# Kernel optimization log

Measured on AMD Instinct MI355X. Metric: run time of the kernel, lower is better.

## Reference

```python
import jax, jax.numpy as jnp
import numpy as np

BATCH = 2048
INPUT_DIM = 512
N = 8 ** 4  # reservoir_n ** reservoir_d = 4096
T = 16
NEG_SLOPE = 0.1
SPARSITY = 0.1  # fraction of nonzero entries in the pre-trained reservoir W


def setup_inputs() -> dict:
    key = jax.random.key(0)
    kx, kw, km = jax.random.split(key, 3)
    x = jax.random.normal(kx, (BATCH, INPUT_DIM), dtype=jnp.float32)
    # Sparse pre-trained reservoir weights; scale keeps spectral norm ~O(1)
    # so the T-step recurrence neither explodes nor vanishes.
    mask = (jax.random.uniform(km, (N, N)) < SPARSITY).astype(jnp.float32)
    W = jax.random.normal(kw, (N, N), dtype=jnp.float32) * mask / jnp.sqrt(SPARSITY * N)
    return {"x": x, "W": W}


def reference(x, W):
    # Pad input [B, input_dim] -> initial state S [B, N]
    S0 = jnp.pad(x, ((0, 0), (0, N - x.shape[1])))

    def step(S, _):
        S = jax.nn.leaky_relu(S @ W, negative_slope=NEG_SLOPE)
        return S, None

    S_final, _ = jax.lax.scan(step, S0, None, length=T)
    return S_final
```

## Files before the change

### kernel.cpp

```cpp
#include <hip/hip_runtime.h>


#define BATCH 2048
#define NDIM  4096
#define INDIM 512
#define BM 128
#define BN 128
#define BK 32

typedef _Float16 f16x8 __attribute__((ext_vector_type(8)));
typedef float    f32x4 __attribute__((ext_vector_type(4)));

__device__ __forceinline__ void async16(const void* gsrc, void* ldst) {
  const __attribute__((address_space(1))) unsigned int* g =
      (const __attribute__((address_space(1))) unsigned int*)gsrc;
  __attribute__((address_space(3))) unsigned int* l =
      (__attribute__((address_space(3))) unsigned int*)ldst;
  __builtin_amdgcn_global_load_lds(g, l, 16, 0, 0);
}

__global__ void prep_x(const float* __restrict__ x,
                       _Float16* __restrict__ Sh, _Float16* __restrict__ Sl) {
  size_t i = (size_t)blockIdx.x * 256 + threadIdx.x;
  int b = (int)(i >> 12);
  int n = (int)(i & (NDIM - 1));
  float v = (n < INDIM) ? x[(size_t)b * INDIM + n] : 0.0f;
  _Float16 h = (_Float16)v;
  Sh[i] = h;
  Sl[i] = (_Float16)(v - (float)h);
}

__global__ void prep_w(const float* __restrict__ W,
                       _Float16* __restrict__ Wth, _Float16* __restrict__ Wtl) {
  __shared__ float tile[32][33];
  int k0 = blockIdx.y * 32, n0 = blockIdx.x * 32;
  int tx = threadIdx.x, ty = threadIdx.y;
  for (int r = 0; r < 4; r++) {
    int k = k0 + ty + r * 8;
    tile[ty + r * 8][tx] = W[(size_t)k * NDIM + n0 + tx];
  }
  __syncthreads();
  for (int r = 0; r < 4; r++) {
    int n = n0 + ty + r * 8;
    float v = tile[tx][ty + r * 8] * 256.0f;
    _Float16 h = (_Float16)v;
    Wth[(size_t)n * NDIM + k0 + tx] = h;
    Wtl[(size_t)n * NDIM + k0 + tx] = (_Float16)(v - (float)h);
  }
}

#define READF(b, A, L, Bv, M)                          \
  do {                                                 \
    _Pragma("unroll") for (int i = 0; i < 4; i++) {    \
      A[i]  = *(const f16x8*)&sAh[b][oA[i]];           \
      L[i]  = *(const f16x8*)&sAl[b][oA[i]];           \
      Bv[i] = *(const f16x8*)&sBh[b][oB[i]];           \
      M[i]  = *(const f16x8*)&sBl[b][oB[i]];           \
    }                                                  \
  } while (0)

#define MFMAS(A, L, Bv, M)                                                          \
  do {                                                                              \
    _Pragma("unroll") for (int j = 0; j < 4; j++)                                   \
    _Pragma("unroll") for (int i = 0; i < 4; i++) {                                 \
      acc[i][j] = __builtin_amdgcn_mfma_f32_16x16x32_f16(A[i], Bv[j], acc[i][j], 0, 0, 0); \
      acc[i][j] = __builtin_amdgcn_mfma_f32_16x16x32_f16(L[i], Bv[j], acc[i][j], 0, 0, 0); \
      acc[i][j] = __builtin_amdgcn_mfma_f32_16x16x32_f16(A[i], M[j], acc[i][j], 0, 0, 0); \
    }                                                                               \
  } while (0)

template <int MODE>
__global__ __launch_bounds__(256, 2) void step_kernel(
    const _Float16* __restrict__ Ah, const _Float16* __restrict__ Al,
    const _Float16* __restrict__ Bh, const _Float16* __restrict__ Bl,
    _Float16* __restrict__ Dh, _Float16* __restrict__ Dl,
    float* __restrict__ Dout, int k_len) {
  __shared__ _Float16 sAh[2][BM * BK];
  __shared__ _Float16 sAl[2][BM * BK];
  __shared__ _Float16 sBh[2][BN * BK];
  __shared__ _Float16 sBl[2][BN * BK];

  const int tid = threadIdx.x;
  const int lane = tid & 63;
  const int w = tid >> 6;
  const int wm = w >> 1, wn = w & 1;

  int id = blockIdx.x;
  int xcd = id & 7, local = id >> 3;
  int lr = local & 7, lc = local >> 3;
  const int bm = ((xcd & 1) * 8 + lr) * BM;
  const int bn = ((xcd >> 1) * 8 + lc) * BN;

  const int sr = lane >> 2, cl = lane & 3;
  const int fm = lane & 15, fq = lane >> 4;

  int oA[4], oB[4];
#pragma unroll
  for (int i = 0; i < 4; i++) {
    int rA = wm * 64 + i * 16 + fm;
    oA[i] = rA * BK + (fq ^ ((rA >> 1) & 3)) * 8;
    int rB = wn * 64 + i * 16 + fm;
    oB[i] = rB * BK + (fq ^ ((rB >> 1) & 3)) * 8;
  }

  int r0 = w * 32 + sr, r1 = r0 + 16;
  int cg0 = cl ^ ((r0 >> 1) & 3);
  int cg1 = cl ^ ((r1 >> 1) & 3);
  const size_t gA0 = (size_t)(bm + r0) * NDIM + cg0 * 8;
  const size_t gA1 = (size_t)(bm + r1) * NDIM + cg1 * 8;
  const size_t gB0 = (size_t)(bn + r0) * NDIM + cg0 * 8;
  const size_t gB1 = (size_t)(bn + r1) * NDIM + cg1 * 8;
  const int lo0 = r0 * BK + cl * 8;
  const int lo1 = r1 * BK + cl * 8;

  auto stage = [&](int kt, int b) {
    async16(Ah + gA0 + kt, &sAh[b][lo0]);
    async16(Ah + gA1 + kt, &sAh[b][lo1]);
    async16(Al + gA0 + kt, &sAl[b][lo0]);
    async16(Al + gA1 + kt, &sAl[b][lo1]);
    async16(Bh + gB0 + kt, &sBh[b][lo0]);
    async16(Bh + gB1 + kt, &sBh[b][lo1]);
    async16(Bl + gB0 + kt, &sBl[b][lo0]);
    async16(Bl + gB1 + kt, &sBl[b][lo1]);
  };

  f32x4 acc[4][4];
#pragma unroll
  for (int i = 0; i < 4; i++)
#pragma unroll
    for (int j = 0; j < 4; j++) acc[i][j] = (f32x4){0.f, 0.f, 0.f, 0.f};

  f16x8 a0[4], l0[4], b0[4], m0[4];
  f16x8 a1[4], l1[4], b1[4], m1[4];

  const int nk = k_len / BK;

  stage(0 * BK, 0);
  stage(1 * BK, 1);
  __syncthreads();
  READF(0, a0, l0, b0, m0);
  __syncthreads();
  stage(2 * BK, 0);

  int it = 1;
  for (; it + 1 < nk; it += 2) {
    READF(1, a1, l1, b1, m1);
    MFMAS(a0, l0, b0, m0);
    __syncthreads();
    if (it + 2 < nk) stage((it + 2) * BK, 1);

    READF(0, a0, l0, b0, m0);
    MFMAS(a1, l1, b1, m1);
    __syncthreads();
    if (it + 3 < nk) stage((it + 3) * BK, 0);
  }
  READF(1, a1, l1, b1, m1);
  MFMAS(a0, l0, b0, m0);
  MFMAS(a1, l1, b1, m1);

  const float inv = 1.0f / 256.0f;
#pragma unroll
  for (int i = 0; i < 4; i++) {
#pragma unroll
    for (int j = 0; j < 4; j++) {
#pragma unroll
      for (int e = 0; e < 4; e++) {
        int r = bm + wm * 64 + i * 16 + fq * 4 + e;
        int c = bn + wn * 64 + j * 16 + fm;
        float g = acc[i][j][e] * inv;
        float s = (g > 0.0f) ? g : 0.1f * g;
        if (MODE == 0) {
          _Float16 h = (_Float16)s;
          Dh[(size_t)r * NDIM + c] = h;
          Dl[(size_t)r * NDIM + c] = (_Float16)(s - (float)h);
        } else {
          Dout[(size_t)r * NDIM + c] = s;
        }
      }
    }
  }
}

extern "C" void kernel_launch(void* const* d_in, const int* in_sizes, int n_in,
                              void* d_out, int out_size, void* d_ws, size_t ws_size,
                              hipStream_t stream) {
  const float* x = (const float*)d_in[0];
  const float* W = (const float*)d_in[1];
  float* out = (float*)d_out;
  char* ws = (char*)d_ws;

  const size_t WT_BYTES = (size_t)NDIM * NDIM * 2;
  const size_t S_BYTES = (size_t)BATCH * NDIM * 2;
  _Float16* Wth = (_Float16*)ws;
  _Float16* Wtl = (_Float16*)(ws + WT_BYTES);
  _Float16* SAh = (_Float16*)(ws + 2 * WT_BYTES);
  _Float16* SAl = (_Float16*)(ws + 2 * WT_BYTES + S_BYTES);
  _Float16* SBh = (_Float16*)(ws + 2 * WT_BYTES + 2 * S_BYTES);
  _Float16* SBl = (_Float16*)(ws + 2 * WT_BYTES + 3 * S_BYTES);

  prep_x<<<(BATCH * NDIM) / 256, 256, 0, stream>>>(x, SAh, SAl);
  prep_w<<<dim3(NDIM / 32, NDIM / 32), dim3(32, 8), 0, stream>>>(W, Wth, Wtl);

  dim3 grid((NDIM / BN) * (BATCH / BM));
  for (int t = 1; t <= 16; t++) {
    const _Float16* ah = (t & 1) ? SAh : SBh;
    const _Float16* al = (t & 1) ? SAl : SBl;
    _Float16* dh = (t & 1) ? SBh : SAh;
    _Float16* dl = (t & 1) ? SBl : SAl;
    int klen = (t == 1) ? INDIM : NDIM;
    if (t < 16)
      step_kernel<0><<<grid, 256, 0, stream>>>(ah, al, Wth, Wtl, dh, dl, nullptr, klen);
    else
      step_kernel<1><<<grid, 256, 0, stream>>>(ah, al, Wth, Wtl, nullptr, nullptr, out, klen);
  }
}
```

Before: 2.418 ms.

## Switch split-fp16 GEMM to 32x32x16 MFMA with k-split LDS layout

Replaces the 16x16x32 MFMA tiling with 32x32x16 MFMA instructions, so each wave computes a 2x2 grid of 32x32 accumulators instead of 4x4 of 16x16. The LDS layout becomes two 16-wide k-slabs per 32-wide k tile, without the XOR swizzle, and the async load addressing and epilogue row/column mapping are rewritten to match. The larger MFMA is meant to raise matrix-core throughput and cut the number of operand fragment loads per FLOP. Dropping the swizzle may add LDS bank conflicts on the fragment reads.

```diff
diff --git a/kernel.cpp b/kernel.cpp
--- a/kernel.cpp
+++ b/kernel.cpp
@@ -8,8 +8,8 @@
 #define BN 128
 #define BK 32
 
-typedef _Float16 f16x8 __attribute__((ext_vector_type(8)));
-typedef float    f32x4 __attribute__((ext_vector_type(4)));
+typedef _Float16 f16x8  __attribute__((ext_vector_type(8)));
+typedef float    f32x16 __attribute__((ext_vector_type(16)));
 
 __device__ __forceinline__ void async16(const void* gsrc, void* ldst) {
   const __attribute__((address_space(1))) unsigned int* g =
@@ -51,22 +51,28 @@
 
 #define READF(b, A, L, Bv, M)                          \
   do {                                                 \
-    _Pragma("unroll") for (int i = 0; i < 4; i++) {    \
-      A[i]  = *(const f16x8*)&sAh[b][oA[i]];           \
-      L[i]  = *(const f16x8*)&sAl[b][oA[i]];           \
-      Bv[i] = *(const f16x8*)&sBh[b][oB[i]];           \
-      M[i]  = *(const f16x8*)&sBl[b][oB[i]];           \
+    _Pragma("unroll") for (int i = 0; i < 2; i++)      \
+    _Pragma("unroll") for (int s = 0; s < 2; s++) {    \
+      A[i][s]  = *(const f16x8*)&sAh[b][oA[i][s]];     \
+      L[i][s]  = *(const f16x8*)&sAl[b][oA[i][s]];     \
+      Bv[i][s] = *(const f16x8*)&sBh[b][oB[i][s]];     \
+      M[i][s]  = *(const f16x8*)&sBl[b][oB[i][s]];     \
     }                                                  \
   } while (0)
 
-#define MFMAS(A, L, Bv, M)                                                          \
-  do {                                                                              \
-    _Pragma("unroll") for (int j = 0; j < 4; j++)                                   \
-    _Pragma("unroll") for (int i = 0; i < 4; i++) {                                 \
-      acc[i][j] = __builtin_amdgcn_mfma_f32_16x16x32_f16(A[i], Bv[j], acc[i][j], 0, 0, 0); \
-      acc[i][j] = __builtin_amdgcn_mfma_f32_16x16x32_f16(L[i], Bv[j], acc[i][j], 0, 0, 0); \
-      acc[i][j] = __builtin_amdgcn_mfma_f32_16x16x32_f16(A[i], M[j], acc[i][j], 0, 0, 0); \
-    }                                                                               \
+#define MFMAS(A, L, Bv, M)                                                                   \
+  do {                                                                                       \
+    _Pragma("unroll") for (int s = 0; s < 2; s++) {                                          \
+      _Pragma("unroll") for (int j = 0; j < 2; j++)                                          \
+      _Pragma("unroll") for (int i = 0; i < 2; i++)                                          \
+        acc[i][j] = __builtin_amdgcn_mfma_f32_32x32x16_f16(A[i][s], Bv[j][s], acc[i][j], 0, 0, 0); \
+      _Pragma("unroll") for (int j = 0; j < 2; j++)                                          \
+      _Pragma("unroll") for (int i = 0; i < 2; i++)                                          \
+        acc[i][j] = __builtin_amdgcn_mfma_f32_32x32x16_f16(L[i][s], Bv[j][s], acc[i][j], 0, 0, 0); \
+      _Pragma("unroll") for (int j = 0; j < 2; j++)                                          \
+      _Pragma("unroll") for (int i = 0; i < 2; i++)                                          \
+        acc[i][j] = __builtin_amdgcn_mfma_f32_32x32x16_f16(A[i][s], M[j][s], acc[i][j], 0, 0, 0); \
+    }                                                                                        \
   } while (0)
 
 template <int MODE>
@@ -75,10 +81,10 @@
     const _Float16* __restrict__ Bh, const _Float16* __restrict__ Bl,
     _Float16* __restrict__ Dh, _Float16* __restrict__ Dl,
     float* __restrict__ Dout, int k_len) {
-  __shared__ _Float16 sAh[2][BM * BK];
-  __shared__ _Float16 sAl[2][BM * BK];
-  __shared__ _Float16 sBh[2][BN * BK];
-  __shared__ _Float16 sBl[2][BN * BK];
+  __shared__ __align__(16) _Float16 sAh[2][2 * BM * 16];
+  __shared__ __align__(16) _Float16 sAl[2][2 * BM * 16];
+  __shared__ __align__(16) _Float16 sBh[2][2 * BN * 16];
+  __shared__ __align__(16) _Float16 sBl[2][2 * BN * 16];
 
   const int tid = threadIdx.x;
   const int lane = tid & 63;
@@ -91,47 +97,49 @@
   const int bm = ((xcd & 1) * 8 + lr) * BM;
   const int bn = ((xcd >> 1) * 8 + lc) * BN;
 
-  const int sr = lane >> 2, cl = lane & 3;
-  const int fm = lane & 15, fq = lane >> 4;
-
-  int oA[4], oB[4];
-#pragma unroll
-  for (int i = 0; i < 4; i++) {
-    int rA = wm * 64 + i * 16 + fm;
-    oA[i] = rA * BK + (fq ^ ((rA >> 1) & 3)) * 8;
-    int rB = wn * 64 + i * 16 + fm;
-    oB[i] = rB * BK + (fq ^ ((rB >> 1) & 3)) * 8;
-  }
-
-  int r0 = w * 32 + sr, r1 = r0 + 16;
-  int cg0 = cl ^ ((r0 >> 1) & 3);
-  int cg1 = cl ^ ((r1 >> 1) & 3);
-  const size_t gA0 = (size_t)(bm + r0) * NDIM + cg0 * 8;
-  const size_t gA1 = (size_t)(bm + r1) * NDIM + cg1 * 8;
-  const size_t gB0 = (size_t)(bn + r0) * NDIM + cg0 * 8;
-  const size_t gB1 = (size_t)(bn + r1) * NDIM + cg1 * 8;
-  const int lo0 = r0 * BK + cl * 8;
-  const int lo1 = r1 * BK + cl * 8;
+  const int r31 = lane & 31;
+  const int kh = lane >> 5;
+
+  int oA[2][2], oB[2][2];
+#pragma unroll
+  for (int i = 0; i < 2; i++)
+#pragma unroll
+    for (int s = 0; s < 2; s++) {
+      oA[i][s] = s * (BM * 16) + (wm * 64 + i * 32 + r31) * 16 + kh * 8;
+      oB[i][s] = s * (BN * 16) + (wn * 64 + i * 32 + r31) * 16 + kh * 8;
+    }
+
+  const int srow = w * 32 + (lane >> 1);
+  const int ksub = (lane & 1) * 8;
+  size_t gA[2], gB[2];
+  int dOff[2];
+#pragma unroll
+  for (int q = 0; q < 2; q++) {
+    gA[q] = (size_t)(bm + srow) * NDIM + q * 16 + ksub;
+    gB[q] = (size_t)(bn + srow) * NDIM + q * 16 + ksub;
+    dOff[q] = q * (BM * 16) + srow * 16 + ksub;
+  }
 
   auto stage = [&](int kt, int b) {
-    async16(Ah + gA0 + kt, &sAh[b][lo0]);
-    async16(Ah + gA1 + kt, &sAh[b][lo1]);
-    async16(Al + gA0 + kt, &sAl[b][lo0]);
-    async16(Al + gA1 + kt, &sAl[b][lo1]);
-    async16(Bh + gB0 + kt, &sBh[b][lo0]);
-    async16(Bh + gB1 + kt, &sBh[b][lo1]);
-    async16(Bl + gB0 + kt, &sBl[b][lo0]);
-    async16(Bl + gB1 + kt, &sBl[b][lo1]);
+#pragma unroll
+    for (int q = 0; q < 2; q++) {
+      async16(Ah + gA[q] + kt, &sAh[b][dOff[q]]);
+      async16(Al + gA[q] + kt, &sAl[b][dOff[q]]);
+      async16(Bh + gB[q] + kt, &sBh[b][dOff[q]]);
+      async16(Bl + gB[q] + kt, &sBl[b][dOff[q]]);
+    }
   };
 
-  f32x4 acc[4][4];
-#pragma unroll
-  for (int i = 0; i < 4; i++)
-#pragma unroll
-    for (int j = 0; j < 4; j++) acc[i][j] = (f32x4){0.f, 0.f, 0.f, 0.f};
-
-  f16x8 a0[4], l0[4], b0[4], m0[4];
-  f16x8 a1[4], l1[4], b1[4], m1[4];
+  f32x16 acc[2][2];
+#pragma unroll
+  for (int i = 0; i < 2; i++)
+#pragma unroll
+    for (int j = 0; j < 2; j++)
+#pragma unroll
+      for (int e = 0; e < 16; e++) acc[i][j][e] = 0.0f;
+
+  f16x8 a0[2][2], l0[2][2], b0[2][2], m0[2][2];
+  f16x8 a1[2][2], l1[2][2], b1[2][2], m1[2][2];
 
   const int nk = k_len / BK;
 
@@ -160,13 +168,13 @@
 
   const float inv = 1.0f / 256.0f;
 #pragma unroll
-  for (int i = 0; i < 4; i++) {
-#pragma unroll
-    for (int j = 0; j < 4; j++) {
-#pragma unroll
-      for (int e = 0; e < 4; e++) {
-        int r = bm + wm * 64 + i * 16 + fq * 4 + e;
-        int c = bn + wn * 64 + j * 16 + fm;
+  for (int i = 0; i < 2; i++) {
+#pragma unroll
+    for (int j = 0; j < 2; j++) {
+#pragma unroll
+      for (int e = 0; e < 16; e++) {
+        int r = bm + wm * 64 + i * 32 + (e & 3) + 8 * (e >> 2) + 4 * kh;
+        int c = bn + wn * 64 + j * 32 + r31;
         float g = acc[i][j][e] * inv;
         float s = (g > 0.0f) ? g : 0.1f * g;
         if (MODE == 0) {
```

Result: slower. 4.178 ms (+72.8%).
